# Kernel optimization log

Measured on AMD Instinct MI355X. Metric: run time of the kernel, lower is better.

Reference implementation:

```python
import jax, jax.numpy as jnp
import numpy as np

B, C, H, W = 2, 128, 128, 256
NW = 4            # len(window_sizes)
CG = C // NW      # channels per attention chunk
EPS = 1e-6
MAXDISP = 192 // 2


def layernorm2d(x, w, b):
    # channel LayerNorm over dim=1 (biased variance), as in LayerNormFunction
    mu = x.mean(axis=1, keepdims=True)
    var = ((x - mu) ** 2).mean(axis=1, keepdims=True)
    y = (x - mu) / jnp.sqrt(var + EPS)
    return w[None, :, None, None] * y + b[None, :, None, None]


def conv1x1(x, w):
    # w: [O, I]
    return jnp.einsum('oi,bihw->bohw', w, x)


def dwconv3(x, w, b):
    # depthwise 3x3, w: [C,1,3,3]
    y = jax.lax.conv_general_dilated(x, w, (1, 1), 'SAME',
                                     feature_group_count=x.shape[1],
                                     dimension_numbers=('NCHW', 'OIHW', 'NCHW'))
    return y + b[None, :, None, None]


def shifts(x):
    # feature shift with n_div=8: 4 groups shifted by 1px in -W,+W,-H,+H, rest identity
    g = x.shape[1] // 8
    padW = lambda a, lo, hi: jnp.pad(a, ((0, 0), (0, 0), (0, 0), (lo, hi)))
    padH = lambda a, lo, hi: jnp.pad(a, ((0, 0), (0, 0), (lo, hi), (0, 0)))
    p0 = padW(x[:, 0 * g:1 * g, :, 1:], 0, 1)   # out[...,:-1] = x[...,1:]
    p1 = padW(x[:, 1 * g:2 * g, :, :-1], 1, 0)  # out[...,1:]  = x[...,:-1]
    p2 = padH(x[:, 2 * g:3 * g, 1:, :], 0, 1)
    p3 = padH(x[:, 3 * g:4 * g, :-1, :], 1, 0)
    return jnp.concatenate([p0, p1, p2, p3, x[:, 4 * g:]], axis=1)


def setup_inputs() -> dict:
    key = jax.random.key(0)
    ks = jax.random.split(key, 12)
    s = 1.0 / np.sqrt(C)
    return {
        'xl0': jax.random.normal(ks[0], (B, C, H, W), jnp.float32),
        'xr0': jax.random.normal(ks[1], (B, C, H, W), jnp.float32),
        'ln_l_w': jnp.ones((C,), jnp.float32),
        'ln_l_b': jnp.zeros((C,), jnp.float32),
        'ln_r_w': jnp.ones((C,), jnp.float32),
        'ln_r_b': jnp.zeros((C,), jnp.float32),
        'feaL_w': jax.random.normal(ks[2], (C, C), jnp.float32) * s,
        'feaR_w': jax.random.normal(ks[3], (C, C), jnp.float32) * s,
        'to_l_w': jax.random.normal(ks[4], (C, C), jnp.float32) * s,
        'to_r_w': jax.random.normal(ks[5], (C, C), jnp.float32) * s,
        'td_w': jax.random.normal(ks[6], (C, 1, 3, 3), jnp.float32) * 0.2,
        'td_b': jnp.zeros((C,), jnp.float32),
        'tp_w': jax.random.normal(ks[7], (C, C), jnp.float32) * s,
        'tp_b': jnp.zeros((C,), jnp.float32),
        'out_w': jax.random.normal(ks[8], (C, C), jnp.float32) * s,
    }


def reference(xl0, xr0, ln_l_w, ln_l_b, ln_r_w, ln_r_b, feaL_w, feaR_w,
              to_l_w, to_r_w, td_w, td_b, tp_w, tp_b, out_w):
    b, c, h, w = xl0.shape
    # values: 1x1 conv on shifted inputs
    vl = conv1x1(shifts(xl0), feaL_w)
    vr = conv1x1(shifts(xr0), feaR_w)

    def transition(x):
        return conv1x1(dwconv3(x, td_w, td_b), tp_w) + tp_b[None, :, None, None]

    x_left = layernorm2d(transition(xl0) + xl0, ln_l_w, ln_l_b)
    x_right = layernorm2d(transition(xr0) + xr0, ln_r_w, ln_r_b)
    ql = conv1x1(shifts(x_left), to_l_w)
    qr = conv1x1(shifts(x_right), to_r_w)

    # split into NW chunks along channels (vectorized over the chunk axis k)
    ql = ql.reshape(b, NW, CG, h, w)
    qr = qr.reshape(b, NW, CG, h, w)
    vl4 = vl.reshape(b, NW, CG, h, w)
    vr4 = vr.reshape(b, NW, CG, h, w)

    # banded disparity mask (multiplicative, as in the torch code):
    # tril(diag=0)*triu(diag=-maxdisp) -> 1 where i-maxdisp <= j <= i
    i = jnp.arange(w)[:, None]
    j = jnp.arange(w)[None, :]
    mask = ((j <= i) & (j >= i - MAXDISP)).astype(xl0.dtype)  # [W, W]

    # per-row cross-view attention over W (no scale: self.scale is unused in forward)
    atn = jnp.einsum('bkchw,bkchv->bkhwv', ql, qr) * mask  # [B,NW,H,W,W]
    warpL = jnp.einsum('bkhwv,bkchv->bkchw', jax.nn.softmax(atn, axis=-1), vr4)
    warpR = jnp.einsum('bkhwv,bkchw->bkchv', jax.nn.softmax(atn, axis=-2), vl4)

    xl = warpL.reshape(b, c, h, w)
    xr = warpR.reshape(b, c, h, w)
    return (conv1x1(xl, out_w) + xl0, conv1x1(xr, out_w) + xr0)
```

## Files before the change

kernel.cpp:

```cpp
#include <hip/hip_runtime.h>

#define DEVI static __device__ __forceinline__

constexpr int B_ = 2, C_ = 128, H_ = 128, W_ = 256;
constexpr int CG_ = 32, MD_ = 96;
constexpr int HW_ = H_ * W_;
constexpr int CHW_ = C_ * HW_;
constexpr int TEN_ = B_ * CHW_;
constexpr int P16_ = TEN_ / 2;

typedef short bf16x8 __attribute__((ext_vector_type(8)));
typedef float f32x16 __attribute__((ext_vector_type(16)));
typedef unsigned short ushort_t;

DEVI ushort_t f2b(float f) {
  unsigned u = __float_as_uint(f);
  return (ushort_t)((u + 0x7fffu + ((u >> 16) & 1u)) >> 16);
}
DEVI unsigned pk2(float a, float b) {
  return (unsigned)f2b(a) | ((unsigned)f2b(b) << 16);
}
DEVI float blo(unsigned u) { return __uint_as_float(u << 16); }
DEVI float bhi(unsigned u) { return __uint_as_float(u & 0xffff0000u); }
DEVI float sum8(uint4 v) {
  return blo(v.x) + bhi(v.x) + blo(v.y) + bhi(v.y) +
         blo(v.z) + bhi(v.z) + blo(v.w) + bhi(v.w);
}
DEVI int xcd_remap(int hw) { return (hw & 7) * 128 + (hw >> 3); }

struct WbPack { const float* s[6]; ushort_t* d[6]; };

__global__ __launch_bounds__(256) void k_wb(WbPack p) {
  int m = blockIdx.y;
  int idx = blockIdx.x * 256 + threadIdx.x;
  p.d[m][idx] = f2b(p.s[m][idx]);
}

DEVI void gemm_core(const unsigned* Xs, const ushort_t* Wb, int lane, int wid,
                    f32x16& acc0, f32x16& acc1) {
  int hi = lane >> 5, lr = lane & 31;
  bf16x8 wf[8];
  const ushort_t* wbase = Wb + (wid * 32 + lr) * 128 + hi * 8;
#pragma unroll
  for (int kk = 0; kk < 8; ++kk) wf[kk] = *(const bf16x8*)(wbase + kk * 16);
  int xsw = lr & 7;
#pragma unroll
  for (int kk = 0; kk < 8; ++kk) {
    int cl = 2 * kk + hi;
    bf16x8 x0 = *(const bf16x8*)&Xs[lr * 64 + ((cl ^ xsw) << 2)];
    bf16x8 x1 = *(const bf16x8*)&Xs[(32 + lr) * 64 + ((cl ^ xsw) << 2)];
    acc0 = __builtin_amdgcn_mfma_f32_32x32x16_bf16(wf[kk], x0, acc0, 0, 0, 0);
    acc1 = __builtin_amdgcn_mfma_f32_32x32x16_bf16(wf[kk], x1, acc1, 0, 0, 0);
  }
}

__global__ __launch_bounds__(256) void k_trans(
    const float* __restrict__ X0, const float* __restrict__ X1,
    const ushort_t* __restrict__ Wb,
    const float* __restrict__ dww, const float* __restrict__ dwb,
    const float* __restrict__ cb,
    const float* __restrict__ lnw0, const float* __restrict__ lnb0,
    const float* __restrict__ lnw1, const float* __restrict__ lnb1,
    unsigned* __restrict__ O0, unsigned* __restrict__ O1) {
  __shared__ __align__(16) unsigned Xs[64 * 64];
  __shared__ float red[640];
  int side = blockIdx.y;
  const float* X = side ? X1 : X0;
  const float* lnw = side ? lnw1 : lnw0;
  const float* lnb = side ? lnb1 : lnb0;
  unsigned* O = side ? O1 : O0;
  int bid = xcd_remap(blockIdx.x);
  int b = bid >> 9, h = (bid >> 2) & 127, w0 = (bid & 3) << 6;
  int t = threadIdx.x;
  int lane = t & 63, wid = t >> 6, hi = lane >> 5, lr = lane & 31;

  int oct = t & 7, cg = t >> 3;
  int wb2 = w0 + oct * 8;
#pragma unroll
  for (int p = 0; p < 2; ++p) {
    float accs[2][8];
#pragma unroll
    for (int cc = 0; cc < 2; ++cc) {
      int c = cg * 4 + p * 2 + cc;
      const float* Xp = X + (b * C_ + c) * HW_;
      const float* wp = dww + c * 9;
      float bb = dwb[c];
#pragma unroll
      for (int i = 0; i < 8; ++i) accs[cc][i] = bb;
#pragma unroll
      for (int dy = -1; dy <= 1; ++dy) {
        int hh = h + dy;
        if (hh < 0 || hh >= H_) continue;
        const float* row = Xp + hh * W_;
        float4 a = *(const float4*)(row + wb2);
        float4 bq = *(const float4*)(row + wb2 + 4);
        float vm = (wb2 > 0) ? row[wb2 - 1] : 0.f;
        float vp = (wb2 + 8 < W_) ? row[wb2 + 8] : 0.f;
        float v10[10] = {vm, a.x, a.y, a.z, a.w, bq.x, bq.y, bq.z, bq.w, vp};
        const float* wr = wp + (dy + 1) * 3;
        float tw0 = wr[0], tw1 = wr[1], tw2 = wr[2];
#pragma unroll
        for (int i = 0; i < 8; ++i) {
          accs[cc][i] += tw0 * v10[i];
          accs[cc][i] += tw1 * v10[i + 1];
          accs[cc][i] += tw2 * v10[i + 2];
        }
      }
    }
    int wic = (2 * cg + p) & 3;
    int clb = cg >> 1;
#pragma unroll
    for (int k = 0; k < 8; ++k) {
      int pxl = (k + oct) & 7;
      int px = oct * 8 + pxl;
      Xs[px * 64 + (((clb ^ pxl) & 15) << 2) + wic] = pk2(accs[0][pxl], accs[1][pxl]);
    }
  }
  __syncthreads();

  f32x16 acc0 = {}, acc1 = {};
  gemm_core(Xs, Wb, lane, wid, acc0, acc1);

  int obase = wid * 32 + 4 * hi;
#pragma unroll
  for (int r = 0; r < 16; ++r) {
    int o = obase + (r & 3) + 8 * (r >> 2);
    float bb = cb[o];
    const float* rp = X + (b * C_ + o) * HW_ + h * W_ + w0;
    acc0[r] += bb + rp[lr];
    acc1[r] += bb + rp[32 + lr];
  }
  {
    float s0 = 0, s1 = 0, q0 = 0, q1 = 0;
#pragma unroll
    for (int r = 0; r < 16; ++r) {
      s0 += acc0[r]; q0 += acc0[r] * acc0[r];
      s1 += acc1[r]; q1 += acc1[r] * acc1[r];
    }
    s0 += __shfl_xor(s0, 32); q0 += __shfl_xor(q0, 32);
    s1 += __shfl_xor(s1, 32); q1 += __shfl_xor(q1, 32);
    if (hi == 0) {
      red[wid * 64 + lr] = s0;       red[wid * 64 + 32 + lr] = s1;
      red[256 + wid * 64 + lr] = q0; red[256 + wid * 64 + 32 + lr] = q1;
    }
    __syncthreads();
    if (t < 64) {
      float ss = red[t] + red[64 + t] + red[128 + t] + red[192 + t];
      float qq = red[256 + t] + red[320 + t] + red[384 + t] + red[448 + t];
      float mu = ss * (1.0f / 128.0f);
      float var = qq * (1.0f / 128.0f) - mu * mu;
      red[512 + t] = mu;
      red[576 + t] = rsqrtf(var + 1e-6f);
    }
    __syncthreads();
    float mu0 = red[512 + lr], rs0 = red[576 + lr];
    float mu1 = red[544 + lr], rs1 = red[608 + lr];
#pragma unroll
    for (int r = 0; r < 16; ++r) {
      int o = obase + (r & 3) + 8 * (r >> 2);
      float lw = lnw[o], lb2 = lnb[o];
      acc0[r] = lw * ((acc0[r] - mu0) * rs0) + lb2;
      acc1[r] = lw * ((acc1[r] - mu1) * rs1) + lb2;
    }
  }
#pragma unroll
  for (int r = 0; r < 16; r += 2) {
    int o = obase + (r & 3) + 8 * (r >> 2);
    unsigned* orow = O + (b * 64 + (o >> 1)) * HW_ + h * W_ + w0;
    orow[lr] = pk2(acc0[r], acc0[r + 1]);
    orow[32 + lr] = pk2(acc1[r], acc1[r + 1]);
  }
}

__global__ __launch_bounds__(256) void k_qv(
    const unsigned* __restrict__ B0, const unsigned* __restrict__ B1,
    const float* __restrict__ X0, const float* __restrict__ X1,
    const ushort_t* __restrict__ WQ0, const ushort_t* __restrict__ WQ1,
    const ushort_t* __restrict__ WV0, const ushort_t* __restrict__ WV1,
    unsigned* __restrict__ Q0, unsigned* __restrict__ Q1,
    unsigned* __restrict__ V0, unsigned* __restrict__ V1) {
  __shared__ __align__(16) unsigned Xs[64 * 64];
  int ty = blockIdx.y;
  int bid = xcd_remap(blockIdx.x);
  int b = bid >> 9, h = (bid >> 2) & 127, w0 = (bid & 3) << 6;
  int t = threadIdx.x;
  int lane = t & 63, wid = t >> 6, hi = lane >> 5, lr = lane & 31;
  const ushort_t* Wb = (ty == 0) ? WQ0 : (ty == 1) ? WQ1 : (ty == 2) ? WV0 : WV1;

  if (ty < 2) {
    const unsigned* S = ty ? B1 : B0;
#pragma unroll
    for (int uu = 0; uu < 4; ++uu) {
      int unit = uu * 256 + t;
      int c2u = unit >> 4, pxq = unit & 15;
      int wb2 = w0 + pxq * 4;
      int g = c2u >> 3;
      unsigned v[4];
      const unsigned* rowp = S + (b * 64 + c2u) * HW_ + h * W_;
      if (g >= 4) {
        uint4 a = *(const uint4*)(rowp + wb2);
        v[0] = a.x; v[1] = a.y; v[2] = a.z; v[3] = a.w;
      } else if (g >= 2) {
        int hh = h + (g == 2 ? 1 : -1);
        if (hh >= 0 && hh < H_) {
          uint4 a = *(const uint4*)(S + (b * 64 + c2u) * HW_ + hh * W_ + wb2);
          v[0] = a.x; v[1] = a.y; v[2] = a.z; v[3] = a.w;
        } else { v[0] = v[1] = v[2] = v[3] = 0u; }
      } else {
        int d = (g == 0) ? 1 : -1;
#pragma unroll
        for (int i = 0; i < 4; ++i) {
          int ww = wb2 + i + d;
          v[i] = (ww >= 0 && ww < W_) ? rowp[ww] : 0u;
        }
      }
#pragma unroll
      for (int i = 0; i < 4; ++i) {
        int px = pxq * 4 + i;
        Xs[px * 64 + (((c2u >> 2) ^ (px & 7)) << 2) + (c2u & 3)] = v[i];
      }
    }
  } else {
    const float* S = (ty == 2) ? X0 : X1;
    int ch8 = t >> 4, pxq = t & 15;
    int c0 = ch8 * 8, wb2 = w0 + pxq * 4;
    float vv[8][4];
#pragma unroll
    for (int cc = 0; cc < 8; ++cc) {
      int c = c0 + cc;
      int g = c >> 4;
      const float* rowp = S + (b * C_ + c) * HW_ + h * W_;
      if (g >= 4) {
        float4 a = *(const float4*)(rowp + wb2);
        vv[cc][0] = a.x; vv[cc][1] = a.y; vv[cc][2] = a.z; vv[cc][3] = a.w;
      } else if (g >= 2) {
        int hh = h + (g == 2 ? 1 : -1);
        if (hh >= 0 && hh < H_) {
          float4 a = *(const float4*)(S + (b * C_ + c) * HW_ + hh * W_ + wb2);
          vv[cc][0] = a.x; vv[cc][1] = a.y; vv[cc][2] = a.z; vv[cc][3] = a.w;
        } else { vv[cc][0] = vv[cc][1] = vv[cc][2] = vv[cc][3] = 0.f; }
      } else if (g == 0) {
        float4 a = *(const float4*)(rowp + wb2);
        float x4 = (wb2 + 4 < W_) ? rowp[wb2 + 4] : 0.f;
        vv[cc][0] = a.y; vv[cc][1] = a.z; vv[cc][2] = a.w; vv[cc][3] = x4;
      } else {
        float4 a = *(const float4*)(rowp + wb2);
        float xm = (wb2 > 0) ? rowp[wb2 - 1] : 0.f;
        vv[cc][0] = xm; vv[cc][1] = a.x; vv[cc][2] = a.y; vv[cc][3] = a.z;
      }
    }
#pragma unroll
    for (int i = 0; i < 4; ++i) {
      int px = pxq * 4 + i;
      int cl = ch8 ^ (px & 7);
      *(uint4*)&Xs[px * 64 + cl * 4] =
          make_uint4(pk2(vv[0][i], vv[1][i]), pk2(vv[2][i], vv[3][i]),
                     pk2(vv[4][i], vv[5][i]), pk2(vv[6][i], vv[7][i]));
    }
  }
  __syncthreads();

  f32x16 acc0 = {}, acc1 = {};
  gemm_core(Xs, Wb, lane, wid, acc0, acc1);

  int obase = wid * 32 + 4 * hi;
  if (ty < 2) {
    unsigned* O = ty ? Q1 : Q0;
#pragma unroll
    for (int r = 0; r < 16; r += 2) {
      int o = obase + (r & 3) + 8 * (r >> 2);
      unsigned* orow = O + b * CHW_ + o * HW_ + h * W_ + w0;
      orow[lr] = pk2(acc0[r], acc0[r + 1]);
      orow[32 + lr] = pk2(acc1[r], acc1[r + 1]);
    }
  } else {
    unsigned* O = (ty == 2) ? V0 : V1;
#pragma unroll
    for (int r = 0; r < 16; r += 2) {
      int o = obase + (r & 3) + 8 * (r >> 2);
      unsigned* orow = O + (b * 64 + (o >> 1)) * HW_ + h * W_ + w0;
      orow[lr] = pk2(acc0[r], acc0[r + 1]);
      orow[32 + lr] = pk2(acc1[r], acc1[r + 1]);
    }
  }
}

DEVI bf16x8 ldfrag(const unsigned* A, int r, int cl) {
  int clp = cl ^ ((r >> 1) & 3);
  uint4 v = *(const uint4*)(A + r * 16 + clp * 4);
  return __builtin_bit_cast(bf16x8, v);
}
DEVI bf16x8 vfrag(const unsigned* Vt, int c, int ktg, int hi) {
  int jc = 2 * ktg + hi;
  int jcp = jc ^ (c & 7);
  uint4 v = *(const uint4*)(Vt + c * 128 + jcp * 4);
  return __builtin_bit_cast(bf16x8, v);
}
DEVI void stageQ16(const unsigned* __restrict__ G, unsigned* A, int t) {
  unsigned r[16];
#pragma unroll
  for (int c2 = 0; c2 < 16; ++c2) r[c2] = G[(2 * c2) * HW_ + t];
  int sw = (t >> 1) & 3;
#pragma unroll
  for (int cl = 0; cl < 4; ++cl) {
    int clp = cl ^ sw;
    *(uint4*)(A + t * 16 + clp * 4) =
        make_uint4(r[cl * 4], r[cl * 4 + 1], r[cl * 4 + 2], r[cl * 4 + 3]);
  }
}
DEVI void stageVt_wr(const unsigned* vbuf, unsigned* Vt, int t) {
  ushort_t* V16 = (ushort_t*)Vt;
#pragma unroll
  for (int c2 = 0; c2 < 16; ++c2) {
    unsigned u = vbuf[c2];
#pragma unroll
    for (int e = 0; e < 2; ++e) {
      int c = 2 * c2 + e;
      int w16 = (c * 128 + (((t >> 3) ^ (c & 7)) << 2) + ((t >> 1) & 3)) * 2 + (t & 1);
      V16[w16] = (ushort_t)(e ? (u >> 16) : (u & 0xffffu));
    }
  }
}
DEVI void stageVt(const unsigned* __restrict__ G, unsigned* Vt, int t) {
  unsigned vbuf[16];
#pragma unroll
  for (int c2 = 0; c2 < 16; ++c2) vbuf[c2] = G[c2 * HW_ + t];
  stageVt_wr(vbuf, Vt, t);
}
DEVI void psv_comp(const unsigned* Vt, float* psv, int t) {
  int jt = t >> 5, c = t & 31;
  float s = 0.f;
#pragma unroll
  for (int q = 0; q < 4; ++q) {
    int jcp = (4 * jt + q) ^ (c & 7);
    s += sum8(*(const uint4*)(Vt + c * 128 + jcp * 4));
  }
  psv[jt * 32 + c] = s;
}

template <int DIR>
DEVI void attn_pass(const unsigned* Ql_, const unsigned* Qk_, const unsigned* Vt,
                    const float* psv, float* emr, unsigned* __restrict__ outG,
                    int wid, int lane) {
  int hi = lane >> 5, cq = lane & 31;
#pragma unroll
  for (int s = 0; s < 2; ++s) {
    int qt = 2 * wid + s;
    int q = qt * 32 + cq;
    int jt0 = DIR ? qt : (qt >= 3 ? qt - 3 : 0);
    int jt1 = DIR ? (qt <= 4 ? qt + 3 : 7) : qt;
    int nt = jt1 - jt0 + 1;
    bf16x8 bq0 = ldfrag(Ql_, q, hi);
    bf16x8 bq1 = ldfrag(Ql_, q, hi + 2);
    f32x16 S[4];
#pragma unroll
    for (int ji = 0; ji < 4; ++ji) {
      if (ji < nt) {
        int jt = jt0 + ji;
        f32x16 d = {};
        d = __builtin_amdgcn_mfma_f32_32x32x16_bf16(
            ldfrag(Qk_, jt * 32 + cq, hi), bq0, d, 0, 0, 0);
        d = __builtin_amdgcn_mfma_f32_32x32x16_bf16(
            ldfrag(Qk_, jt * 32 + cq, hi + 2), bq1, d, 0, 0, 0);
        S[ji] = d;
      }
    }
    float m = 0.f;
#pragma unroll
    for (int ji = 0; ji < 4; ++ji) if (ji < nt) {
      int jb = (jt0 + ji) * 32 + 4 * hi;
#pragma unroll
      for (int r = 0; r < 16; ++r) {
        int j = jb + (r & 3) + 8 * (r >> 2);
        bool act = DIR ? (j >= q && j <= q + MD_) : (j <= q && j >= q - MD_);
        float v = act ? S[ji][r] : 0.f;
        S[ji][r] = v;
        m = fmaxf(m, v);
      }
    }
    m = fmaxf(m, __shfl_xor(m, 32));
    float em_ = __expf(-m);
    float lsum = 0.f;
#pragma unroll
    for (int ji = 0; ji < 4; ++ji) if (ji < nt) {
#pragma unroll
      for (int r = 0; r < 16; ++r) {
        float e = __expf(S[ji][r] - m);
        S[ji][r] = e;
        lsum += e;
      }
    }
    lsum += __shfl_xor(lsum, 32);
    lsum += (float)((8 - nt) * 32) * em_;
    float rl = 1.f / lsum;
    if (hi == 0) { emr[qt * 32 + cq] = em_; emr[256 + qt * 32 + cq] = rl; }
    f32x16 acc = {};
#pragma unroll
    for (int ji = 0; ji < 4; ++ji) if (ji < nt) {
      int jt = jt0 + ji;
      unsigned x[8], ox[8];
#pragma unroll
      for (int w2 = 0; w2 < 8; ++w2) x[w2] = pk2(S[ji][2 * w2], S[ji][2 * w2 + 1]);
#pragma unroll
      for (int w2 = 0; w2 < 8; ++w2) ox[w2] = __shfl_xor(x[w2], 32);
#pragma unroll
      for (int hf = 0; hf < 2; ++hf) {
        unsigned w0 = hi ? ox[4 * hf + 2] : x[4 * hf + 0];
        unsigned w1 = hi ? ox[4 * hf + 3] : x[4 * hf + 1];
        unsigned w2_ = hi ? x[4 * hf + 2] : ox[4 * hf + 0];
        unsigned w3 = hi ? x[4 * hf + 3] : ox[4 * hf + 1];
        uint4 aw = make_uint4(w0, w1, w2_, w3);
        acc = __builtin_amdgcn_mfma_f32_32x32x16_bf16(
            __builtin_bit_cast(bf16x8, aw), vfrag(Vt, cq, 2 * jt + hf, hi),
            acc, 0, 0, 0);
      }
    }
    float Rv = 0.f;
#pragma unroll
    for (int jt = 0; jt < 8; ++jt)
      if (jt < jt0 || jt > jt1) Rv += psv[jt * 32 + cq];
#pragma unroll
    for (int r = 0; r < 16; r += 2) {
      int qr0 = (r & 3) + 8 * (r >> 2) + 4 * hi;
      float v0 = (acc[r] + emr[qt * 32 + qr0] * Rv) * emr[256 + qt * 32 + qr0];
      float v1 = (acc[r + 1] + emr[qt * 32 + qr0 + 1] * Rv) * emr[256 + qt * 32 + qr0 + 1];
      outG[cq * (HW_ / 2) + ((qt * 32 + qr0) >> 1)] = pk2(v0, v1);
    }
  }
}

__global__ __launch_bounds__(256) void k_attn(
    const unsigned* __restrict__ qL, const unsigned* __restrict__ qR,
    const unsigned* __restrict__ vL, const unsigned* __restrict__ vR,
    unsigned* __restrict__ wL, unsigned* __restrict__ wR) {
  __shared__ __align__(16) unsigned Ql[4096];
  __shared__ __align__(16) unsigned Qr[4096];
  __shared__ __align__(16) unsigned Vt[4096];
  __shared__ float psv[256];
  __shared__ float emr[512];
  int t = threadIdx.x;
  int bid = blockIdx.x;
  int b = bid >> 9, k4 = (bid >> 7) & 3, h = bid & 127;
  int qoff = b * CHW_ + (k4 * CG_) * HW_ + h * W_;
  int voff = (b * 64 + k4 * 16) * HW_ + h * W_;
  int woff = (b * C_ + k4 * CG_) * (HW_ / 2) + h * (W_ / 2);
  stageQ16(qL + qoff, Ql, t);
  stageQ16(qR + qoff, Qr, t);
  stageVt(vR + voff, Vt, t);
  __syncthreads();
  psv_comp(Vt, psv, t);
  __syncthreads();
  int wid = t >> 6, lane = t & 63;
  unsigned vbuf[16];
  {
    const unsigned* G = vL + voff;
#pragma unroll
    for (int c2 = 0; c2 < 16; ++c2) vbuf[c2] = G[c2 * HW_ + t];
  }
  attn_pass<0>(Ql, Qr, Vt, psv, emr, wL + woff, wid, lane);
  __syncthreads();
  stageVt_wr(vbuf, Vt, t);
  __syncthreads();
  psv_comp(Vt, psv, t);
  __syncthreads();
  attn_pass<1>(Qr, Ql, Vt, psv, emr, wR + woff, wid, lane);
}

__global__ __launch_bounds__(256) void k_fin(
    const unsigned* __restrict__ W0, const unsigned* __restrict__ W1,
    const float* __restrict__ X0, const float* __restrict__ X1,
    const ushort_t* __restrict__ Wb,
    float* __restrict__ O0, float* __restrict__ O1) {
  __shared__ __align__(16) unsigned Xs[64 * 64];
  int side = blockIdx.y;
  const unsigned* Wsrc = side ? W1 : W0;
  const float* R = side ? X1 : X0;
  float* O = side ? O1 : O0;
  int bid = blockIdx.x;
  int b = bid >> 9, h = (bid >> 2) & 127, w0 = (bid & 3) << 6;
  int t = threadIdx.x;
  int lane = t & 63, wid = t >> 6, hi = lane >> 5, lr = lane & 31;
#pragma unroll
  for (int uu = 0; uu < 8; ++uu) {
    int unit = uu * 256 + t;
    int cp = unit >> 5;
    int jp = unit & 31;
    const unsigned* base = Wsrc + h * (W_ / 2) + (w0 >> 1) + jp;
    unsigned lo = base[(b * C_ + 2 * cp) * (HW_ / 2)];
    unsigned hi2 = base[(b * C_ + 2 * cp + 1) * (HW_ / 2)];
    unsigned w0p = (lo & 0xffffu) | (hi2 << 16);
    unsigned w1p = (lo >> 16) | (hi2 & 0xffff0000u);
    int px0 = 2 * jp, px1 = 2 * jp + 1;
    Xs[px0 * 64 + (((cp >> 2) ^ (px0 & 7)) << 2) + (cp & 3)] = w0p;
    Xs[px1 * 64 + (((cp >> 2) ^ (px1 & 7)) << 2) + (cp & 3)] = w1p;
  }
  __syncthreads();
  f32x16 acc0 = {}, acc1 = {};
  gemm_core(Xs, Wb, lane, wid, acc0, acc1);
  int obase = wid * 32 + 4 * hi;
#pragma unroll
  for (int r = 0; r < 16; ++r) {
    int o = obase + (r & 3) + 8 * (r >> 2);
    const float* rp = R + (b * C_ + o) * HW_ + h * W_ + w0;
    float* op = O + (b * C_ + o) * HW_ + h * W_ + w0;
    op[lr] = acc0[r] + rp[lr];
    op[32 + lr] = acc1[r] + rp[32 + lr];
  }
}

extern "C" void kernel_launch(void* const* d_in, const int* in_sizes, int n_in,
                              void* d_out, int out_size, void* d_ws, size_t ws_size,
                              hipStream_t stream) {
  const float* xl0    = (const float*)d_in[0];
  const float* xr0    = (const float*)d_in[1];
  const float* ln_l_w = (const float*)d_in[2];
  const float* ln_l_b = (const float*)d_in[3];
  const float* ln_r_w = (const float*)d_in[4];
  const float* ln_r_b = (const float*)d_in[5];
  const float* feaL_w = (const float*)d_in[6];
  const float* feaR_w = (const float*)d_in[7];
  const float* to_l_w = (const float*)d_in[8];
  const float* to_r_w = (const float*)d_in[9];
  const float* td_w   = (const float*)d_in[10];
  const float* td_b   = (const float*)d_in[11];
  const float* tp_w   = (const float*)d_in[12];
  const float* tp_b   = (const float*)d_in[13];
  const float* out_w  = (const float*)d_in[14];

  float* o0 = (float*)d_out;
  float* o1 = o0 + TEN_;
  unsigned* qL = (unsigned*)d_out;
  unsigned* qR = qL + TEN_;
  unsigned* bL = (unsigned*)d_ws;
  unsigned* bR = bL + P16_;
  unsigned* vL = bR + P16_;
  unsigned* vR = vL + P16_;
  ushort_t* wb = (ushort_t*)(vR + P16_);
  ushort_t* wb_feaL = wb + 0 * 16384;
  ushort_t* wb_feaR = wb + 1 * 16384;
  ushort_t* wb_tol  = wb + 2 * 16384;
  ushort_t* wb_tor  = wb + 3 * 16384;
  ushort_t* wb_tp   = wb + 4 * 16384;
  ushort_t* wb_out  = wb + 5 * 16384;

  WbPack pw;
  pw.s[0] = feaL_w; pw.s[1] = feaR_w; pw.s[2] = to_l_w;
  pw.s[3] = to_r_w; pw.s[4] = tp_w;   pw.s[5] = out_w;
  pw.d[0] = wb_feaL; pw.d[1] = wb_feaR; pw.d[2] = wb_tol;
  pw.d[3] = wb_tor;  pw.d[4] = wb_tp;   pw.d[5] = wb_out;
  k_wb<<<dim3(64, 6), 256, 0, stream>>>(pw);

  k_trans<<<dim3(1024, 2), 256, 0, stream>>>(
      xl0, xr0, wb_tp, td_w, td_b, tp_b,
      ln_l_w, ln_l_b, ln_r_w, ln_r_b, bL, bR);

  k_qv<<<dim3(1024, 4), 256, 0, stream>>>(
      bL, bR, xl0, xr0, wb_tol, wb_tor, wb_feaL, wb_feaR,
      qL, qR, vL, vR);

  k_attn<<<1024, 256, 0, stream>>>(qL, qR, vL, vR, bL, bR);

  k_fin<<<dim3(1024, 2), 256, 0, stream>>>(
      bL, bR, xl0, xr0, wb_out, o0, o1);
}
```

Measured before the change: 188.3 us.

## Process two rows per block in transition kernel to reuse depthwise input rows

Each k_trans block now handles two adjacent image rows instead of one. The depthwise 3x3 reads four input rows instead of six, and the bf16 weight fragments are loaded once and reused for both rows' MFMA GEMMs. The grid is halved to 512x2 blocks with a matching XCD remap. LDS use doubles, register pressure rises from the doubled accumulators, and the second row's epilogue runs behind an extra barrier, which may cut occupancy and the number of blocks in flight.

```diff
diff --git a/kernel.cpp b/kernel.cpp
--- a/kernel.cpp
+++ b/kernel.cpp
@@ -27,6 +27,7 @@
          blo(v.z) + bhi(v.z) + blo(v.w) + bhi(v.w);
 }
 DEVI int xcd_remap(int hw) { return (hw & 7) * 128 + (hw >> 3); }
+DEVI int xcd_remap512(int hw) { return (hw & 7) * 64 + (hw >> 3); }
 
 struct WbPack { const float* s[6]; ushort_t* d[6]; };
 
@@ -62,15 +63,16 @@
     const float* __restrict__ lnw0, const float* __restrict__ lnb0,
     const float* __restrict__ lnw1, const float* __restrict__ lnb1,
     unsigned* __restrict__ O0, unsigned* __restrict__ O1) {
-  __shared__ __align__(16) unsigned Xs[64 * 64];
+  __shared__ __align__(16) unsigned Xs[2][64 * 64];
   __shared__ float red[640];
   int side = blockIdx.y;
   const float* X = side ? X1 : X0;
   const float* lnw = side ? lnw1 : lnw0;
   const float* lnb = side ? lnb1 : lnb0;
   unsigned* O = side ? O1 : O0;
-  int bid = xcd_remap(blockIdx.x);
-  int b = bid >> 9, h = (bid >> 2) & 127, w0 = (bid & 3) << 6;
+  int bid = xcd_remap512(blockIdx.x);
+  int b = bid >> 8, hp = (bid >> 2) & 63, w0 = (bid & 3) << 6;
+  int h0 = hp * 2;
   int t = threadIdx.x;
   int lane = t & 63, wid = t >> 6, hi = lane >> 5, lr = lane & 31;
 
@@ -78,7 +80,7 @@
   int wb2 = w0 + oct * 8;
 #pragma unroll
   for (int p = 0; p < 2; ++p) {
-    float accs[2][8];
+    float accs[2][2][8];
 #pragma unroll
     for (int cc = 0; cc < 2; ++cc) {
       int c = cg * 4 + p * 2 + cc;
@@ -86,10 +88,10 @@
       const float* wp = dww + c * 9;
       float bb = dwb[c];
 #pragma unroll
-      for (int i = 0; i < 8; ++i) accs[cc][i] = bb;
-#pragma unroll
-      for (int dy = -1; dy <= 1; ++dy) {
-        int hh = h + dy;
+      for (int i = 0; i < 8; ++i) { accs[0][cc][i] = bb; accs[1][cc][i] = bb; }
+#pragma unroll
+      for (int r = 0; r < 4; ++r) {
+        int hh = h0 - 1 + r;
         if (hh < 0 || hh >= H_) continue;
         const float* row = Xp + hh * W_;
         float4 a = *(const float4*)(row + wb2);
@@ -97,78 +99,110 @@
         float vm = (wb2 > 0) ? row[wb2 - 1] : 0.f;
         float vp = (wb2 + 8 < W_) ? row[wb2 + 8] : 0.f;
         float v10[10] = {vm, a.x, a.y, a.z, a.w, bq.x, bq.y, bq.z, bq.w, vp};
-        const float* wr = wp + (dy + 1) * 3;
-        float tw0 = wr[0], tw1 = wr[1], tw2 = wr[2];
-#pragma unroll
-        for (int i = 0; i < 8; ++i) {
-          accs[cc][i] += tw0 * v10[i];
-          accs[cc][i] += tw1 * v10[i + 1];
-          accs[cc][i] += tw2 * v10[i + 2];
+        if (r <= 2) {
+          const float* wr = wp + r * 3;
+          float tw0 = wr[0], tw1 = wr[1], tw2 = wr[2];
+#pragma unroll
+          for (int i = 0; i < 8; ++i) {
+            accs[0][cc][i] += tw0 * v10[i];
+            accs[0][cc][i] += tw1 * v10[i + 1];
+            accs[0][cc][i] += tw2 * v10[i + 2];
+          }
+        }
+        if (r >= 1) {
+          const float* wr = wp + (r - 1) * 3;
+          float tw0 = wr[0], tw1 = wr[1], tw2 = wr[2];
+#pragma unroll
+          for (int i = 0; i < 8; ++i) {
+            accs[1][cc][i] += tw0 * v10[i];
+            accs[1][cc][i] += tw1 * v10[i + 1];
+            accs[1][cc][i] += tw2 * v10[i + 2];
+          }
         }
       }
     }
     int wic = (2 * cg + p) & 3;
     int clb = cg >> 1;
 #pragma unroll
-    for (int k = 0; k < 8; ++k) {
-      int pxl = (k + oct) & 7;
-      int px = oct * 8 + pxl;
-      Xs[px * 64 + (((clb ^ pxl) & 15) << 2) + wic] = pk2(accs[0][pxl], accs[1][pxl]);
-    }
-  }
-  __syncthreads();
-
-  f32x16 acc0 = {}, acc1 = {};
-  gemm_core(Xs, Wb, lane, wid, acc0, acc1);
-
+    for (int tr = 0; tr < 2; ++tr)
+#pragma unroll
+      for (int k = 0; k < 8; ++k) {
+        int pxl = (k + oct) & 7;
+        int px = oct * 8 + pxl;
+        Xs[tr][px * 64 + (((clb ^ pxl) & 15) << 2) + wic] =
+            pk2(accs[tr][0][pxl], accs[tr][1][pxl]);
+      }
+  }
+  __syncthreads();
+
+  bf16x8 wf[8];
+  const ushort_t* wbase = Wb + (wid * 32 + lr) * 128 + hi * 8;
+#pragma unroll
+  for (int kk = 0; kk < 8; ++kk) wf[kk] = *(const bf16x8*)(wbase + kk * 16);
+  int xsw = lr & 7;
   int obase = wid * 32 + 4 * hi;
-#pragma unroll
-  for (int r = 0; r < 16; ++r) {
-    int o = obase + (r & 3) + 8 * (r >> 2);
-    float bb = cb[o];
-    const float* rp = X + (b * C_ + o) * HW_ + h * W_ + w0;
-    acc0[r] += bb + rp[lr];
-    acc1[r] += bb + rp[32 + lr];
-  }
-  {
-    float s0 = 0, s1 = 0, q0 = 0, q1 = 0;
-#pragma unroll
-    for (int r = 0; r < 16; ++r) {
-      s0 += acc0[r]; q0 += acc0[r] * acc0[r];
-      s1 += acc1[r]; q1 += acc1[r] * acc1[r];
-    }
-    s0 += __shfl_xor(s0, 32); q0 += __shfl_xor(q0, 32);
-    s1 += __shfl_xor(s1, 32); q1 += __shfl_xor(q1, 32);
-    if (hi == 0) {
-      red[wid * 64 + lr] = s0;       red[wid * 64 + 32 + lr] = s1;
-      red[256 + wid * 64 + lr] = q0; red[256 + wid * 64 + 32 + lr] = q1;
-    }
-    __syncthreads();
-    if (t < 64) {
-      float ss = red[t] + red[64 + t] + red[128 + t] + red[192 + t];
-      float qq = red[256 + t] + red[320 + t] + red[384 + t] + red[448 + t];
-      float mu = ss * (1.0f / 128.0f);
-      float var = qq * (1.0f / 128.0f) - mu * mu;
-      red[512 + t] = mu;
-      red[576 + t] = rsqrtf(var + 1e-6f);
-    }
-    __syncthreads();
-    float mu0 = red[512 + lr], rs0 = red[576 + lr];
-    float mu1 = red[544 + lr], rs1 = red[608 + lr];
+
+#pragma unroll
+  for (int tr = 0; tr < 2; ++tr) {
+    if (tr) __syncthreads();
+    int h = h0 + tr;
+    f32x16 acc0 = {}, acc1 = {};
+#pragma unroll
+    for (int kk = 0; kk < 8; ++kk) {
+      int cl = 2 * kk + hi;
+      bf16x8 x0 = *(const bf16x8*)&Xs[tr][lr * 64 + ((cl ^ xsw) << 2)];
+      bf16x8 x1 = *(const bf16x8*)&Xs[tr][(32 + lr) * 64 + ((cl ^ xsw) << 2)];
+      acc0 = __builtin_amdgcn_mfma_f32_32x32x16_bf16(wf[kk], x0, acc0, 0, 0, 0);
+      acc1 = __builtin_amdgcn_mfma_f32_32x32x16_bf16(wf[kk], x1, acc1, 0, 0, 0);
+    }
 #pragma unroll
     for (int r = 0; r < 16; ++r) {
       int o = obase + (r & 3) + 8 * (r >> 2);
-      float lw = lnw[o], lb2 = lnb[o];
-      acc0[r] = lw * ((acc0[r] - mu0) * rs0) + lb2;
-      acc1[r] = lw * ((acc1[r] - mu1) * rs1) + lb2;
-    }
-  }
-#pragma unroll
-  for (int r = 0; r < 16; r += 2) {
-    int o = obase + (r & 3) + 8 * (r >> 2);
-    unsigned* orow = O + (b * 64 + (o >> 1)) * HW_ + h * W_ + w0;
-    orow[lr] = pk2(acc0[r], acc0[r + 1]);
-    orow[32 + lr] = pk2(acc1[r], acc1[r + 1]);
+      float bb = cb[o];
+      const float* rp = X + (b * C_ + o) * HW_ + h * W_ + w0;
+      acc0[r] += bb + rp[lr];
+      acc1[r] += bb + rp[32 + lr];
+    }
+    {
+      float s0 = 0, s1 = 0, q0 = 0, q1 = 0;
+#pragma unroll
+      for (int r = 0; r < 16; ++r) {
+        s0 += acc0[r]; q0 += acc0[r] * acc0[r];
+        s1 += acc1[r]; q1 += acc1[r] * acc1[r];
+      }
+      s0 += __shfl_xor(s0, 32); q0 += __shfl_xor(q0, 32);
+      s1 += __shfl_xor(s1, 32); q1 += __shfl_xor(q1, 32);
+      if (hi == 0) {
+        red[wid * 64 + lr] = s0;       red[wid * 64 + 32 + lr] = s1;
+        red[256 + wid * 64 + lr] = q0; red[256 + wid * 64 + 32 + lr] = q1;
+      }
+      __syncthreads();
+      if (t < 64) {
+        float ss = red[t] + red[64 + t] + red[128 + t] + red[192 + t];
+        float qq = red[256 + t] + red[320 + t] + red[384 + t] + red[448 + t];
+        float mu = ss * (1.0f / 128.0f);
+        float var = qq * (1.0f / 128.0f) - mu * mu;
+        red[512 + t] = mu;
+        red[576 + t] = rsqrtf(var + 1e-6f);
+      }
+      __syncthreads();
+      float mu0 = red[512 + lr], rs0 = red[576 + lr];
+      float mu1 = red[544 + lr], rs1 = red[608 + lr];
+#pragma unroll
+      for (int r = 0; r < 16; ++r) {
+        int o = obase + (r & 3) + 8 * (r >> 2);
+        float lw = lnw[o], lb2 = lnb[o];
+        acc0[r] = lw * ((acc0[r] - mu0) * rs0) + lb2;
+        acc1[r] = lw * ((acc1[r] - mu1) * rs1) + lb2;
+      }
+    }
+#pragma unroll
+    for (int r = 0; r < 16; r += 2) {
+      int o = obase + (r & 3) + 8 * (r >> 2);
+      unsigned* orow = O + (b * 64 + (o >> 1)) * HW_ + h * W_ + w0;
+      orow[lr] = pk2(acc0[r], acc0[r + 1]);
+      orow[32 + lr] = pk2(acc1[r], acc1[r + 1]);
+    }
   }
 }
 
@@ -550,7 +584,7 @@
   pw.d[3] = wb_tor;  pw.d[4] = wb_tp;   pw.d[5] = wb_out;
   k_wb<<<dim3(64, 6), 256, 0, stream>>>(pw);
 
-  k_trans<<<dim3(1024, 2), 256, 0, stream>>>(
+  k_trans<<<dim3(512, 2), 256, 0, stream>>>(
       xl0, xr0, wb_tp, td_w, td_b, tp_b,
       ln_l_w, ln_l_b, ln_r_w, ln_r_b, bL, bR);
 
```

New measurement: 200.4 us. +6.4%, slower.
